# Optimization experiments

Measured on AMD Instinct MI355X. Metric: run time of the kernel, lower is better.

The kernel has to match this reference:

```python
import jax, jax.numpy as jnp
import numpy as np

B, S, IN, D, H, L, F = 4, 1024, 6, 512, 8, 4, 2048
DK = D // H
EPS = 1e-5

def _pos_encoding(S, D):
    pos = np.arange(S, dtype=np.float32)[:, None]
    div = np.exp(np.arange(0, D, 2, dtype=np.float32) * (-np.log(10000.0) / D))
    pe = np.zeros((S, D), np.float32)
    pe[:, 0::2] = np.sin(pos * div)
    pe[:, 1::2] = np.cos(pos * div)
    return jnp.asarray(pe)

def setup_inputs() -> dict:
    key = jax.random.key(0)
    ks = jax.random.split(key, 12)
    def w(k, shape):
        return jax.random.normal(k, shape, jnp.float32) * 0.02
    return {
        "left_wrist": jax.random.normal(ks[0], (B, S, IN), jnp.float32),
        "right_wrist": jax.random.normal(ks[1], (B, S, IN), jnp.float32),
        "Wl": w(ks[2], (IN, D)), "bl": jnp.zeros((D,), jnp.float32),
        "Wr": w(ks[3], (IN, D)), "br": jnp.zeros((D,), jnp.float32),
        "pe": _pos_encoding(S, D),
        # 4 attention blocks per layer (cross1to2, cross2to1, self1, self2), each with q/k/v/o projections
        "mha_w": w(ks[4], (L, 4, 4, D, D)), "mha_b": jnp.zeros((L, 4, 4, D), jnp.float32),
        "mha_ln_g": jnp.ones((L, 4, D), jnp.float32), "mha_ln_b": jnp.zeros((L, 4, D), jnp.float32),
        # 2 FFNs per layer (channel 1 / channel 2)
        "ff_w1": w(ks[5], (L, 2, D, F)), "ff_b1": jnp.zeros((L, 2, F), jnp.float32),
        "ff_w2": w(ks[6], (L, 2, F, D)), "ff_b2": jnp.zeros((L, 2, D), jnp.float32),
        "ff_ln_g": jnp.ones((L, 2, D), jnp.float32), "ff_ln_b": jnp.zeros((L, 2, D), jnp.float32),
        "h1_w1": w(ks[7], (2 * D, D)), "h1_b1": jnp.zeros((D,), jnp.float32),
        "h1_w2": w(ks[8], (D, 2)), "h1_b2": jnp.zeros((2,), jnp.float32),
        "h2_w1": w(ks[9], (2 * D, D)), "h2_b1": jnp.zeros((D,), jnp.float32),
        "h2_w2": w(ks[10], (D, 2)), "h2_b2": jnp.zeros((2,), jnp.float32),
    }

def _ln(x, g, b):
    m = jnp.mean(x, axis=-1, keepdims=True)
    v = jnp.var(x, axis=-1, keepdims=True)
    return (x - m) * jax.lax.rsqrt(v + EPS) * g + b

def _mha(q_in, k_in, v_in, w, b, g, beta):
    # w: [4, D, D] for q/k/v/o, b: [4, D]
    def proj(x, i):
        return (x @ w[i] + b[i]).reshape(x.shape[0], x.shape[1], H, DK).transpose(0, 2, 1, 3)
    Q, K, V = proj(q_in, 0), proj(k_in, 1), proj(v_in, 2)
    scores = jnp.einsum('bhqd,bhkd->bhqk', Q, K) * np.float32(1.0 / np.sqrt(DK))
    attn = jax.nn.softmax(scores, axis=-1)
    ctx = jnp.einsum('bhqk,bhkd->bhqd', attn, V)
    ctx = ctx.transpose(0, 2, 1, 3).reshape(q_in.shape[0], q_in.shape[1], D)
    out = ctx @ w[3] + b[3]
    return _ln(out + q_in, g, beta)

def _ffn(x, w1, b1, w2, b2, g, beta):
    h = jax.nn.relu(x @ w1 + b1)
    return _ln(h @ w2 + b2 + x, g, beta)

def reference(left_wrist, right_wrist, Wl, bl, Wr, br, pe,
              mha_w, mha_b, mha_ln_g, mha_ln_b,
              ff_w1, ff_b1, ff_w2, ff_b2, ff_ln_g, ff_ln_b,
              h1_w1, h1_b1, h1_w2, h1_b2, h2_w1, h2_b1, h2_w2, h2_b2):
    left = left_wrist @ Wl + bl + pe[None]
    right = right_wrist @ Wr + br + pe[None]
    for l in range(L):
        lc = _mha(left, right, right, mha_w[l, 0], mha_b[l, 0], mha_ln_g[l, 0], mha_ln_b[l, 0])
        rc = _mha(right, left, left, mha_w[l, 1], mha_b[l, 1], mha_ln_g[l, 1], mha_ln_b[l, 1])
        ls = _mha(lc, lc, lc, mha_w[l, 2], mha_b[l, 2], mha_ln_g[l, 2], mha_ln_b[l, 2])
        rs = _mha(rc, rc, rc, mha_w[l, 3], mha_b[l, 3], mha_ln_g[l, 3], mha_ln_b[l, 3])
        left = _ffn(ls, ff_w1[l, 0], ff_b1[l, 0], ff_w2[l, 0], ff_b2[l, 0], ff_ln_g[l, 0], ff_ln_b[l, 0])
        right = _ffn(rs, ff_w1[l, 1], ff_b1[l, 1], ff_w2[l, 1], ff_b2[l, 1], ff_ln_g[l, 1], ff_ln_b[l, 1])
    # AdaptiveAvgPool1d(1) over seq == mean over seq axis
    fused = jnp.concatenate([jnp.mean(left, axis=1), jnp.mean(right, axis=1)], axis=1)  # [B, 2D]
    logits1 = jax.nn.relu(fused @ h1_w1 + h1_b1) @ h1_w2 + h1_b2
    logits2 = jax.nn.relu(fused @ h2_w1 + h2_b1) @ h2_w2 + h2_b2
    return (logits1, logits2)
```

## Files before the change

kernel.cpp:

```cpp
#include <hip/hip_runtime.h>
#include <hip/hip_bf16.h>

#define NB 4
#define NS 1024
#define NIN 6
#define ND 512
#define NH 8
#define NLAYERS 4
#define NF 2048
#define NDK 64
#define LN_EPS 1e-5f

typedef unsigned short u16;
typedef __attribute__((ext_vector_type(4))) unsigned short u16x4;
typedef __attribute__((ext_vector_type(8))) short s16x8;
typedef __attribute__((ext_vector_type(4))) float f32x4;
typedef __attribute__((ext_vector_type(4))) unsigned int u32x4;

#define MFMA_BF16(A, B, C) __builtin_amdgcn_mfma_f32_16x16x32_bf16(A, B, C, 0, 0, 0)

#define GLOAD_LDS16(gsrc, ldst)                                                  \
    __builtin_amdgcn_global_load_lds(                                            \
        (const __attribute__((address_space(1))) void*)(gsrc),                   \
        (__attribute__((address_space(3))) void*)(ldst), 16, 0, 0)

__device__ inline u16 f2bf(float f) {
    __bf16 h = (__bf16)f;
    return __builtin_bit_cast(u16, h);
}
__device__ inline float bf2f(u16 v) {
    unsigned int u = (unsigned int)v << 16;
    return __builtin_bit_cast(float, u);
}

__global__ __launch_bounds__(256) void transpose_kernel(
    const float* __restrict__ src, u16* __restrict__ dst, int K, int N) {
    __shared__ u16 t[64][72];
    const int tid = threadIdx.x;
    src += (size_t)blockIdx.z * K * N;
    dst += (size_t)blockIdx.z * K * N;
    const int n0 = blockIdx.x * 64, k0 = blockIdx.y * 64;
    {
        int r = tid >> 2, cq = (tid & 3) * 16;
        const float* sp = src + (size_t)(k0 + r) * N + n0 + cq;
#pragma unroll
        for (int q = 0; q < 4; ++q) {
            float4 v = *reinterpret_cast<const float4*>(sp + q * 4);
            t[r][cq + q * 4 + 0] = f2bf(v.x);
            t[r][cq + q * 4 + 1] = f2bf(v.y);
            t[r][cq + q * 4 + 2] = f2bf(v.z);
            t[r][cq + q * 4 + 3] = f2bf(v.w);
        }
    }
    __syncthreads();
    {
        int rn = tid >> 2, cq = (tid & 3) * 16;
        s16x8 o0, o1;
#pragma unroll
        for (int j = 0; j < 8; ++j) o0[j] = (short)t[cq + j][rn];
#pragma unroll
        for (int j = 0; j < 8; ++j) o1[j] = (short)t[cq + 8 + j][rn];
        u16* dp = dst + (size_t)(n0 + rn) * K + k0 + cq;
        *reinterpret_cast<s16x8*>(dp) = o0;
        *reinterpret_cast<s16x8*>(dp + 8) = o1;
    }
}

__global__ __launch_bounds__(256) void in_proj_kernel(
    const float* __restrict__ x, const float* __restrict__ W,
    const float* __restrict__ bias, const float* __restrict__ pe,
    float* __restrict__ out, u16* __restrict__ outb) {
    int idx = blockIdx.x * 256 + threadIdx.x;
    int d = idx & (ND - 1);
    int bs = idx / ND;
    int s = bs & (NS - 1);
    const float* xr = x + (size_t)bs * NIN;
    float acc = bias[d] + pe[(size_t)s * ND + d];
#pragma unroll
    for (int i = 0; i < NIN; ++i) acc += xr[i] * W[(size_t)i * ND + d];
    out[idx] = acc;
    outb[idx] = f2bf(acc);
}

template <int BN>
__device__ inline void gemm_core(const u16* __restrict__ A, const u16* __restrict__ Wt,
                                 int K, int bm, int bn, char* lds, int tid,
                                 f32x4 (&acc)[4][BN / 32]) {
    constexpr int NT = BN / 32;
    constexpr int ASZ = 128 * 128;
    constexpr int BSZ = BN * 128;
    const int wid = tid >> 6, lane = tid & 63;
    const int l15 = lane & 15, lhi = lane >> 4;
    const int wr = wid >> 1, wc = wid & 1;

    auto stage = [&](int buf, int k0) {
#pragma unroll
        for (int i = 0; i < 4; ++i) {
            int slot = (wid * 4 + i) * 64 + lane;
            int r = slot >> 3, p = slot & 7;
            const char* src = (const char*)(A + (size_t)(bm + r) * K + k0)
                              + ((p * 16) ^ ((r & 7) << 4));
            GLOAD_LDS16(src, lds + buf * ASZ + (wid * 4 + i) * 1024);
        }
#pragma unroll
        for (int i = 0; i < BN / 32; ++i) {
            int slot = (wid * (BN / 32) + i) * 64 + lane;
            int r = slot >> 3, p = slot & 7;
            const char* src = (const char*)(Wt + (size_t)(bn + r) * K + k0)
                              + ((p * 16) ^ ((r & 7) << 4));
            GLOAD_LDS16(src, lds + 2 * ASZ + buf * BSZ + (wid * (BN / 32) + i) * 1024);
        }
    };

#pragma unroll
    for (int mt = 0; mt < 4; ++mt)
#pragma unroll
        for (int nt = 0; nt < NT; ++nt) acc[mt][nt] = f32x4{0.f, 0.f, 0.f, 0.f};

    const int KT = K >> 6;
    stage(0, 0);
    __syncthreads();
    for (int t = 0; t < KT; ++t) {
        if (t + 1 < KT) stage((t + 1) & 1, (t + 1) << 6);
        const char* Ab = lds + (t & 1) * ASZ;
        const char* Bb = lds + 2 * ASZ + (t & 1) * BSZ;
#pragma unroll
        for (int sl = 0; sl < 2; ++sl) {
            s16x8 af[4];
#pragma unroll
            for (int mt = 0; mt < 4; ++mt) {
                int row = wr * 64 + mt * 16 + l15;
                af[mt] = *reinterpret_cast<const s16x8*>(
                    Ab + ((row * 128 + sl * 64 + lhi * 16) ^ ((row & 7) << 4)));
            }
            s16x8 bfr[NT];
#pragma unroll
            for (int nt = 0; nt < NT; ++nt) {
                int row = wc * (BN / 2) + nt * 16 + l15;
                bfr[nt] = *reinterpret_cast<const s16x8*>(
                    Bb + ((row * 128 + sl * 64 + lhi * 16) ^ ((row & 7) << 4)));
            }
#pragma unroll
            for (int mt = 0; mt < 4; ++mt)
#pragma unroll
                for (int nt = 0; nt < NT; ++nt)
                    acc[mt][nt] = MFMA_BF16(af[mt], bfr[nt], acc[mt][nt]);
        }
        __syncthreads();
    }
}

template <int OMODE, int BN>
__global__ __launch_bounds__(256) void bgemm2_kernel(
    const u16* __restrict__ a0, const u16* __restrict__ a1,
    const u16* __restrict__ wt0, const u16* __restrict__ wt1,
    const float* __restrict__ bias0, const float* __restrict__ bias1,
    u16* __restrict__ Cv, int M, int N, int K) {
    constexpr int NT = BN / 32;
    __shared__ char lds[2 * 128 * 128 + 2 * BN * 128];
    const int tid = threadIdx.x, z = blockIdx.z;
    const int bm = blockIdx.y * 128, bn = blockIdx.x * BN;
    const u16* A = z ? a1 : a0;
    const u16* Wt = z ? wt1 : wt0;
    const float* bias = z ? bias1 : bias0;

    f32x4 acc[4][NT];
    gemm_core<BN>(A, Wt, K, bm, bn, lds, tid, acc);

    const int wid = tid >> 6, lane = tid & 63;
    const int l15 = lane & 15, lhi = lane >> 4;
    const int wr = wid >> 1, wc = wid & 1;
    float bv[NT];
#pragma unroll
    for (int nt = 0; nt < NT; ++nt) bv[nt] = bias[bn + wc * (BN / 2) + nt * 16 + l15];

    u16* C = Cv + (size_t)z * M * N;
#pragma unroll
    for (int mt = 0; mt < 4; ++mt) {
        int m0 = bm + wr * 64 + mt * 16 + lhi * 4;
#pragma unroll
        for (int nt = 0; nt < NT; ++nt) {
            int n = bn + wc * (BN / 2) + nt * 16 + l15;
#pragma unroll
            for (int r = 0; r < 4; ++r) {
                float v = acc[mt][nt][r] + bv[nt];
                if (OMODE == 1) v = fmaxf(v, 0.f);
                C[(size_t)(m0 + r) * N + n] = f2bf(v);
            }
        }
    }
}

__global__ __launch_bounds__(256) void bgemm_qkv_kernel(
    const u16* __restrict__ aq0, const u16* __restrict__ aq1,
    const u16* __restrict__ akv0, const u16* __restrict__ akv1,
    const u16* __restrict__ wt0, const u16* __restrict__ wt1,
    const float* __restrict__ bb0, const float* __restrict__ bb1,
    u16* __restrict__ Qo, u16* __restrict__ Ko, u16* __restrict__ Vto) {
    __shared__ char lds[2 * 128 * 128 + 2 * 64 * 128];
    const int tid = threadIdx.x, z = blockIdx.z;
    const int proj = blockIdx.x >> 3;
    const int bm = blockIdx.y * 128, bn = (blockIdx.x & 7) * 64;
    const int M = NB * NS;
    const u16* A = (proj == 0) ? (z ? aq1 : aq0) : (z ? akv1 : akv0);
    const u16* Wt = (z ? wt1 : wt0) + (size_t)proj * ND * ND;
    const float* bias = (z ? bb1 : bb0) + proj * ND;

    f32x4 acc[4][2];
    gemm_core<64>(A, Wt, ND, bm, bn, lds, tid, acc);

    const int wid = tid >> 6, lane = tid & 63;
    const int l15 = lane & 15, lhi = lane >> 4;
    const int wr = wid >> 1, wc = wid & 1;
    float bv[2];
#pragma unroll
    for (int nt = 0; nt < 2; ++nt) bv[nt] = bias[bn + wc * 32 + nt * 16 + l15];

    if (proj < 2) {
        u16* C = (proj ? Ko : Qo) + (size_t)z * M * ND;
#pragma unroll
        for (int mt = 0; mt < 4; ++mt) {
            int m0 = bm + wr * 64 + mt * 16 + lhi * 4;
#pragma unroll
            for (int nt = 0; nt < 2; ++nt) {
                int n = bn + wc * 32 + nt * 16 + l15;
#pragma unroll
                for (int r = 0; r < 4; ++r)
                    C[(size_t)(m0 + r) * ND + n] = f2bf(acc[mt][nt][r] + bv[nt]);
            }
        }
    } else {
#pragma unroll
        for (int mt = 0; mt < 4; ++mt) {
            int m0 = bm + wr * 64 + mt * 16 + lhi * 4;
            int b = (z * M + m0) >> 10, s = m0 & (NS - 1);
#pragma unroll
            for (int nt = 0; nt < 2; ++nt) {
                int n = bn + wc * 32 + nt * 16 + l15;
                int h = n >> 6, dk = n & 63;
                u16x4 o = {f2bf(acc[mt][nt][0] + bv[nt]), f2bf(acc[mt][nt][1] + bv[nt]),
                           f2bf(acc[mt][nt][2] + bv[nt]), f2bf(acc[mt][nt][3] + bv[nt])};
                *reinterpret_cast<u16x4*>(Vto + ((size_t)((b * NH + h) * NDK + dk)) * NS + s) = o;
            }
        }
    }
}

__global__ __launch_bounds__(256) void ln2_kernel(
    const u16* __restrict__ x, const float* __restrict__ res,
    const float* __restrict__ g0, const float* __restrict__ g1,
    const float* __restrict__ be0, const float* __restrict__ be1,
    float* __restrict__ outf, u16* __restrict__ outb) {
    const int wid = threadIdx.x >> 6, lane = threadIdx.x & 63;
    const int row = blockIdx.x * 4 + wid;
    const float* g = (row >> 12) ? g1 : g0;
    const float* be = (row >> 12) ? be1 : be0;
    const int c0 = lane * 8;
    const size_t base = (size_t)row * ND + c0;

    u32x4 xp = *reinterpret_cast<const u32x4*>(x + base);
    float4 ra = *reinterpret_cast<const float4*>(res + base);
    float4 rb = *reinterpret_cast<const float4*>(res + base + 4);
    float v[8];
    v[0] = bf2f((u16)(xp[0] & 0xffffu)) + ra.x;
    v[1] = bf2f((u16)(xp[0] >> 16)) + ra.y;
    v[2] = bf2f((u16)(xp[1] & 0xffffu)) + ra.z;
    v[3] = bf2f((u16)(xp[1] >> 16)) + ra.w;
    v[4] = bf2f((u16)(xp[2] & 0xffffu)) + rb.x;
    v[5] = bf2f((u16)(xp[2] >> 16)) + rb.y;
    v[6] = bf2f((u16)(xp[3] & 0xffffu)) + rb.z;
    v[7] = bf2f((u16)(xp[3] >> 16)) + rb.w;

    float s = 0.f, sq = 0.f;
#pragma unroll
    for (int i = 0; i < 8; ++i) { s += v[i]; sq += v[i] * v[i]; }
#pragma unroll
    for (int m = 1; m < 64; m <<= 1) { s += __shfl_xor(s, m); sq += __shfl_xor(sq, m); }
    float mean = s * (1.f / ND);
    float var = sq * (1.f / ND) - mean * mean;
    float rstd = rsqrtf(var + LN_EPS);

    float4 ga = *reinterpret_cast<const float4*>(g + c0);
    float4 gb = *reinterpret_cast<const float4*>(g + c0 + 4);
    float4 ba = *reinterpret_cast<const float4*>(be + c0);
    float4 bb = *reinterpret_cast<const float4*>(be + c0 + 4);
    float gg[8] = {ga.x, ga.y, ga.z, ga.w, gb.x, gb.y, gb.z, gb.w};
    float bbv[8] = {ba.x, ba.y, ba.z, ba.w, bb.x, bb.y, bb.z, bb.w};
    float o[8];
#pragma unroll
    for (int i = 0; i < 8; ++i) o[i] = (v[i] - mean) * rstd * gg[i] + bbv[i];

    float4 oa = {o[0], o[1], o[2], o[3]};
    float4 ob = {o[4], o[5], o[6], o[7]};
    *reinterpret_cast<float4*>(outf + base) = oa;
    *reinterpret_cast<float4*>(outf + base + 4) = ob;
    u32x4 pk;
#pragma unroll
    for (int i = 0; i < 4; ++i)
        pk[i] = (unsigned int)f2bf(o[2 * i]) | ((unsigned int)f2bf(o[2 * i + 1]) << 16);
    *reinterpret_cast<u32x4*>(outb + base) = pk;
}

__global__ __launch_bounds__(256, 4) void attn_kernel(
    const u16* __restrict__ Qb, const u16* __restrict__ Kb,
    const u16* __restrict__ Vtb, u16* __restrict__ O) {
    __shared__ u16 Ks[128 * 64];
    __shared__ u16 Vts[64 * 128];
    __shared__ u16 Ps[4][16 * 64];

    const int tid = threadIdx.x;
    const int w = tid >> 6, lane = tid & 63;
    const int l15 = lane & 15, lhi = lane >> 4;
    const int bh = blockIdx.y;
    const int b = bh >> 3, h = bh & 7;
    const int qb = blockIdx.x * 64 + w * 16;
    const float c1 = 0.18033688011f;

    s16x8 qf[2];
    {
        const u16* qp = Qb + ((size_t)(b * NS) + qb + l15) * ND + h * NDK + lhi * 8;
        qf[0] = *reinterpret_cast<const s16x8*>(qp);
        qf[1] = *reinterpret_cast<const s16x8*>(qp + 32);
    }

    f32x4 o[4] = {f32x4{0.f, 0.f, 0.f, 0.f}, f32x4{0.f, 0.f, 0.f, 0.f},
                  f32x4{0.f, 0.f, 0.f, 0.f}, f32x4{0.f, 0.f, 0.f, 0.f}};
    float m = -1e30f;
    float lsum = 0.f;

    const u16* Kbase = Kb + ((size_t)(b * NS)) * ND + h * NDK;
    const u16* Vbase = Vtb + ((size_t)bh * NDK) * NS;

    for (int c = 0; c < NS / 128; ++c) {
        const int kv0 = c * 128;
        __syncthreads();
#pragma unroll
        for (int i = 0; i < 4; ++i) {
            int slot = (w * 4 + i) * 64 + lane;
            {
                int r = slot >> 3, p = slot & 7;
                const char* src = (const char*)(Kbase + (size_t)(kv0 + r) * ND)
                                  + ((p ^ (r & 7)) * 16);
                GLOAD_LDS16(src, (char*)Ks + (w * 4 + i) * 1024);
            }
            {
                int r = slot >> 4, p = slot & 15;
                const char* src = (const char*)(Vbase + (size_t)r * NS + kv0)
                                  + ((p ^ (r & 7)) * 16);
                GLOAD_LDS16(src, (char*)Vts + (w * 4 + i) * 1024);
            }
        }
        __syncthreads();

        f32x4 sc[8];
#pragma unroll
        for (int blk = 0; blk < 8; ++blk) sc[blk] = f32x4{0.f, 0.f, 0.f, 0.f};
#pragma unroll
        for (int sl = 0; sl < 2; ++sl) {
#pragma unroll
            for (int blk = 0; blk < 8; ++blk) {
                int krow = blk * 16 + l15;
                s16x8 kf = *reinterpret_cast<const s16x8*>((char*)Ks +
                    ((krow * 128 + sl * 64 + lhi * 16) ^ ((krow & 7) << 4)));
                sc[blk] = MFMA_BF16(kf, qf[sl], sc[blk]);
            }
        }
        float mx = -1e30f;
#pragma unroll
        for (int blk = 0; blk < 8; ++blk)
#pragma unroll
            for (int r = 0; r < 4; ++r) mx = fmaxf(mx, sc[blk][r]);
        mx = fmaxf(mx, __shfl_xor(mx, 16));
        mx = fmaxf(mx, __shfl_xor(mx, 32));
        float mn = fmaxf(m, mx);
        if (__any((mn - m) * c1 > 8.f)) {
            float corr = exp2f((m - mn) * c1);
            m = mn;
            lsum *= corr;
            float cO[4];
#pragma unroll
            for (int r = 0; r < 4; ++r) cO[r] = __shfl(corr, lhi * 4 + r);
#pragma unroll
            for (int db = 0; db < 4; ++db)
#pragma unroll
                for (int r = 0; r < 4; ++r) o[db][r] *= cO[r];
        }
        float d = m * c1;
        float rs = 0.f;
#pragma unroll
        for (int blk = 0; blk < 8; ++blk) {
#pragma unroll
            for (int r = 0; r < 4; ++r) {
                float p = exp2f(fmaf(sc[blk][r], c1, -d));
                sc[blk][r] = p;
                rs += p;
            }
        }
        rs += __shfl_xor(rs, 16);
        rs += __shfl_xor(rs, 32);
        lsum += rs;

#pragma unroll
        for (int hh = 0; hh < 2; ++hh) {
#pragma unroll
            for (int bl = 0; bl < 4; ++bl) {
                int blk = hh * 4 + bl;
                u16x4 pk = {f2bf(sc[blk][0]), f2bf(sc[blk][1]),
                            f2bf(sc[blk][2]), f2bf(sc[blk][3])};
                *reinterpret_cast<u16x4*>((char*)(Ps[w]) +
                    ((l15 * 128 + bl * 32 + lhi * 8) ^ ((l15 & 7) << 4))) = pk;
            }
#pragma unroll
            for (int sl2 = 0; sl2 < 2; ++sl2) {
                s16x8 pf = *reinterpret_cast<const s16x8*>((char*)(Ps[w]) +
                    ((l15 * 128 + sl2 * 64 + lhi * 16) ^ ((l15 & 7) << 4)));
                int ss = hh * 2 + sl2;
#pragma unroll
                for (int db = 0; db < 4; ++db) {
                    int vr = db * 16 + l15;
                    s16x8 vf = *reinterpret_cast<const s16x8*>((char*)Vts +
                        ((vr * 256 + ss * 64 + lhi * 16) ^ ((vr & 7) << 4)));
                    o[db] = MFMA_BF16(pf, vf, o[db]);
                }
            }
        }
    }
    float lsO[4];
#pragma unroll
    for (int r = 0; r < 4; ++r) lsO[r] = __shfl(lsum, lhi * 4 + r);
#pragma unroll
    for (int db = 0; db < 4; ++db) {
#pragma unroll
        for (int r = 0; r < 4; ++r) {
            int q = qb + lhi * 4 + r;
            O[((size_t)(b * NS) + q) * ND + h * NDK + db * 16 + l15] =
                f2bf(o[db][r] / lsO[r]);
        }
    }
}

__global__ __launch_bounds__(256) void pool2_kernel(
    const float* __restrict__ RES, float* __restrict__ fused) {
    const int b = blockIdx.x, half = blockIdx.y, sc = blockIdx.z;
    const size_t NTOK = (size_t)NB * NS * ND;
    const float* src = RES + (half ? NTOK : 0) + ((size_t)(b * NS + sc * 128)) * ND;
    const int tid = threadIdx.x;
#pragma unroll
    for (int cc = 0; cc < 2; ++cc) {
        int c = cc * 256 + tid;
        float s = 0.f;
        for (int r = 0; r < 128; ++r) s += src[(size_t)r * ND + c];
        atomicAdd(&fused[b * 1024 + half * 512 + c], s * (1.f / NS));
    }
}

__global__ __launch_bounds__(256) void head_hidden_kernel(
    const float* __restrict__ fused,
    const float* __restrict__ w1a, const float* __restrict__ b1a,
    const float* __restrict__ w1b, const float* __restrict__ b1b,
    float* __restrict__ hid) {
    const int b = blockIdx.x >> 1, head = blockIdx.x & 1;
    const float* w1 = head ? w1b : w1a;
    const float* b1 = head ? b1b : b1a;
    const int tid = threadIdx.x;
    const int j = blockIdx.y * 64 + (tid & 63);
    const int kq = tid >> 6;
    const float* fr = fused + (size_t)b * (2 * ND);
    float p = 0.f;
    for (int k = kq * 256; k < kq * 256 + 256; ++k)
        p += fr[k] * w1[(size_t)k * ND + j];
    __shared__ float part[4][64];
    part[kq][tid & 63] = p;
    __syncthreads();
    if (tid < 64) {
        float v = part[0][tid] + part[1][tid] + part[2][tid] + part[3][tid] + b1[j];
        hid[(size_t)blockIdx.x * ND + j] = fmaxf(v, 0.f);
    }
}

__global__ __launch_bounds__(256) void head_out_kernel(
    const float* __restrict__ hid,
    const float* __restrict__ w2a, const float* __restrict__ b2a,
    const float* __restrict__ w2b, const float* __restrict__ b2b,
    float* __restrict__ out) {
    const int b = blockIdx.x >> 1, head = blockIdx.x & 1;
    const float* w2 = head ? w2b : w2a;
    const float* b2 = head ? b2b : b2a;
    const int tid = threadIdx.x;
    const float* hr = hid + (size_t)blockIdx.x * ND;
    float h0 = hr[tid], h1 = hr[tid + 256];
    float p0 = h0 * w2[tid * 2 + 0] + h1 * w2[(tid + 256) * 2 + 0];
    float p1 = h0 * w2[tid * 2 + 1] + h1 * w2[(tid + 256) * 2 + 1];
#pragma unroll
    for (int m = 1; m < 64; m <<= 1) { p0 += __shfl_xor(p0, m); p1 += __shfl_xor(p1, m); }
    __shared__ float r0s[4], r1s[4];
    int wid = tid >> 6, lane = tid & 63;
    if (lane == 0) { r0s[wid] = p0; r1s[wid] = p1; }
    __syncthreads();
    if (tid == 0) {
        out[head * 8 + b * 2 + 0] = r0s[0] + r0s[1] + r0s[2] + r0s[3] + b2[0];
        out[head * 8 + b * 2 + 1] = r1s[0] + r1s[1] + r1s[2] + r1s[3] + b2[1];
    }
}

extern "C" void kernel_launch(void* const* d_in, const int* in_sizes, int n_in,
                              void* d_out, int out_size, void* d_ws, size_t ws_size,
                              hipStream_t stream) {
    const float* left_wrist  = (const float*)d_in[0];
    const float* right_wrist = (const float*)d_in[1];
    const float* Wl = (const float*)d_in[2];
    const float* bl = (const float*)d_in[3];
    const float* Wr = (const float*)d_in[4];
    const float* br = (const float*)d_in[5];
    const float* pe = (const float*)d_in[6];
    const float* mha_w    = (const float*)d_in[7];
    const float* mha_b    = (const float*)d_in[8];
    const float* mha_ln_g = (const float*)d_in[9];
    const float* mha_ln_b = (const float*)d_in[10];
    const float* ff_w1 = (const float*)d_in[11];
    const float* ff_b1 = (const float*)d_in[12];
    const float* ff_w2 = (const float*)d_in[13];
    const float* ff_b2 = (const float*)d_in[14];
    const float* ff_ln_g = (const float*)d_in[15];
    const float* ff_ln_b = (const float*)d_in[16];
    const float* h1_w1 = (const float*)d_in[17];
    const float* h1_b1 = (const float*)d_in[18];
    const float* h1_w2 = (const float*)d_in[19];
    const float* h1_b2 = (const float*)d_in[20];
    const float* h2_w1 = (const float*)d_in[21];
    const float* h2_b1 = (const float*)d_in[22];
    const float* h2_w2 = (const float*)d_in[23];
    const float* h2_b2 = (const float*)d_in[24];
    float* out = (float*)d_out;

    const size_t NTOK = (size_t)NB * NS * ND;
    const int M = NB * NS;
    float* ws = (float*)d_ws;
    float* RES   = ws;
    float* CRES  = RES + 2 * NTOK;
    float* TMPf  = CRES + 2 * NTOK;
    float* FUSED = TMPf + 2 * NTOK;
    float* HID   = FUSED + NB * 2 * ND;
    u16* TMPbf = (u16*)TMPf;
    u16* Xbf  = (u16*)(HID + 8 * ND);
    u16* CXbf = Xbf + 2 * NTOK;
    u16* Qbf  = CXbf + 2 * NTOK;
    u16* Kbf  = Qbf + 2 * NTOK;
    u16* Vtbf = Kbf + 2 * NTOK;
    u16* CTbf = Vtbf + 2 * NTOK;
    u16* Hh   = Qbf;
    u16* WtM  = CTbf + 2 * NTOK;
    u16* WtF1 = WtM + (size_t)64 * ND * ND;
    u16* WtF2 = WtF1 + (size_t)8 * ND * NF;

    const size_t DD = (size_t)ND * ND;

    transpose_kernel<<<dim3(ND / 64, ND / 64, 64), 256, 0, stream>>>(mha_w, WtM, ND, ND);
    transpose_kernel<<<dim3(NF / 64, ND / 64, 8), 256, 0, stream>>>(ff_w1, WtF1, ND, NF);
    transpose_kernel<<<dim3(ND / 64, NF / 64, 8), 256, 0, stream>>>(ff_w2, WtF2, NF, ND);

    in_proj_kernel<<<(NB * NS * ND) / 256, 256, 0, stream>>>(left_wrist, Wl, bl, pe, RES, Xbf);
    in_proj_kernel<<<(NB * NS * ND) / 256, 256, 0, stream>>>(right_wrist, Wr, br, pe,
                                                             RES + NTOK, Xbf + NTOK);

    for (int l = 0; l < NLAYERS; ++l) {
        const u16* wt0 = WtM + ((size_t)l * 4 + 0) * 4 * DD;
        const u16* wt1 = WtM + ((size_t)l * 4 + 1) * 4 * DD;
        const u16* wt2 = WtM + ((size_t)l * 4 + 2) * 4 * DD;
        const u16* wt3 = WtM + ((size_t)l * 4 + 3) * 4 * DD;
        const float* bb0 = mha_b + ((size_t)l * 4 + 0) * 4 * ND;
        const float* bb1 = mha_b + ((size_t)l * 4 + 1) * 4 * ND;
        const float* bb2 = mha_b + ((size_t)l * 4 + 2) * 4 * ND;
        const float* bb3 = mha_b + ((size_t)l * 4 + 3) * 4 * ND;

        bgemm_qkv_kernel<<<dim3(24, 32, 2), 256, 0, stream>>>(
            Xbf, Xbf + NTOK, Xbf + NTOK, Xbf, wt0, wt1, bb0, bb1, Qbf, Kbf, Vtbf);
        attn_kernel<<<dim3(NS / 64, 2 * NB * NH), 256, 0, stream>>>(Qbf, Kbf, Vtbf, CTbf);
        bgemm2_kernel<2, 64><<<dim3(8, 32, 2), 256, 0, stream>>>(
            CTbf, CTbf + NTOK, wt0 + 3 * DD, wt1 + 3 * DD, bb0 + 3 * ND, bb1 + 3 * ND,
            TMPbf, M, ND, ND);
        ln2_kernel<<<2 * M / 4, 256, 0, stream>>>(
            TMPbf, RES, mha_ln_g + ((size_t)l * 4 + 0) * ND, mha_ln_g + ((size_t)l * 4 + 1) * ND,
            mha_ln_b + ((size_t)l * 4 + 0) * ND, mha_ln_b + ((size_t)l * 4 + 1) * ND,
            CRES, CXbf);

        bgemm_qkv_kernel<<<dim3(24, 32, 2), 256, 0, stream>>>(
            CXbf, CXbf + NTOK, CXbf, CXbf + NTOK, wt2, wt3, bb2, bb3, Qbf, Kbf, Vtbf);
        attn_kernel<<<dim3(NS / 64, 2 * NB * NH), 256, 0, stream>>>(Qbf, Kbf, Vtbf, CTbf);
        bgemm2_kernel<2, 64><<<dim3(8, 32, 2), 256, 0, stream>>>(
            CTbf, CTbf + NTOK, wt2 + 3 * DD, wt3 + 3 * DD, bb2 + 3 * ND, bb3 + 3 * ND,
            TMPbf, M, ND, ND);
        ln2_kernel<<<2 * M / 4, 256, 0, stream>>>(
            TMPbf, CRES, mha_ln_g + ((size_t)l * 4 + 2) * ND, mha_ln_g + ((size_t)l * 4 + 3) * ND,
            mha_ln_b + ((size_t)l * 4 + 2) * ND, mha_ln_b + ((size_t)l * 4 + 3) * ND,
            RES, Xbf);

        bgemm2_kernel<1, 128><<<dim3(16, 32, 2), 256, 0, stream>>>(
            Xbf, Xbf + NTOK, WtF1 + ((size_t)l * 2 + 0) * ND * NF, WtF1 + ((size_t)l * 2 + 1) * ND * NF,
            ff_b1 + ((size_t)l * 2 + 0) * NF, ff_b1 + ((size_t)l * 2 + 1) * NF,
            Hh, M, NF, ND);
        bgemm2_kernel<2, 64><<<dim3(8, 32, 2), 256, 0, stream>>>(
            Hh, Hh + (size_t)M * NF, WtF2 + ((size_t)l * 2 + 0) * NF * ND, WtF2 + ((size_t)l * 2 + 1) * NF * ND,
            ff_b2 + ((size_t)l * 2 + 0) * ND, ff_b2 + ((size_t)l * 2 + 1) * ND,
            TMPbf, M, ND, NF);
        ln2_kernel<<<2 * M / 4, 256, 0, stream>>>(
            TMPbf, RES, ff_ln_g + ((size_t)l * 2 + 0) * ND, ff_ln_g + ((size_t)l * 2 + 1) * ND,
            ff_ln_b + ((size_t)l * 2 + 0) * ND, ff_ln_b + ((size_t)l * 2 + 1) * ND,
            RES, Xbf);
    }

    hipMemsetAsync(FUSED, 0, NB * 2 * ND * sizeof(float), stream);
    pool2_kernel<<<dim3(NB, 2, 8), 256, 0, stream>>>(RES, FUSED);
    head_hidden_kernel<<<dim3(8, 8), 256, 0, stream>>>(FUSED, h1_w1, h1_b1, h2_w1, h2_b1, HID);
    head_out_kernel<<<8, 256, 0, stream>>>(HID, h1_w2, h1_b2, h2_w2, h2_b2, out);
}
```

Before: 1.320 ms.

## Widen attention blocks to 8 waves, remap grid, and stage output through LDS

The attention kernel now runs 512 threads (8 waves, 128 queries per block), so each K/V chunk loaded into LDS is shared by twice as many query rows. The 1-D grid index is remapped so that consecutive blocks land on different batch-head pairs, which is likely meant to spread load across XCDs or L2 slices. The output is written into the per-wave P buffer first and then stored as 16-byte row-contiguous vectors instead of scattered 2-byte stores. The cost is fewer blocks (512) and higher per-block LDS and register pressure.

```diff
diff --git a/kernel.cpp b/kernel.cpp
--- a/kernel.cpp
+++ b/kernel.cpp
@@ -301,19 +301,21 @@
     *reinterpret_cast<u32x4*>(outb + base) = pk;
 }
 
-__global__ __launch_bounds__(256, 4) void attn_kernel(
+__global__ __launch_bounds__(512, 6) void attn_kernel(
     const u16* __restrict__ Qb, const u16* __restrict__ Kb,
     const u16* __restrict__ Vtb, u16* __restrict__ O) {
     __shared__ u16 Ks[128 * 64];
     __shared__ u16 Vts[64 * 128];
-    __shared__ u16 Ps[4][16 * 64];
+    __shared__ u16 Ps[8][16 * 64];
 
     const int tid = threadIdx.x;
     const int w = tid >> 6, lane = tid & 63;
     const int l15 = lane & 15, lhi = lane >> 4;
-    const int bh = blockIdx.y;
+    const int i0 = blockIdx.x;
+    const int qx = (i0 >> 3) & 7;
+    const int bh = (i0 & 7) * 8 + (i0 >> 6);
     const int b = bh >> 3, h = bh & 7;
-    const int qb = blockIdx.x * 64 + w * 16;
+    const int qb = qx * 128 + w * 16;
     const float c1 = 0.18033688011f;
 
     s16x8 qf[2];
@@ -335,19 +337,19 @@
         const int kv0 = c * 128;
         __syncthreads();
 #pragma unroll
-        for (int i = 0; i < 4; ++i) {
-            int slot = (w * 4 + i) * 64 + lane;
+        for (int i = 0; i < 2; ++i) {
+            int slot = i * 512 + tid;
             {
                 int r = slot >> 3, p = slot & 7;
                 const char* src = (const char*)(Kbase + (size_t)(kv0 + r) * ND)
                                   + ((p ^ (r & 7)) * 16);
-                GLOAD_LDS16(src, (char*)Ks + (w * 4 + i) * 1024);
+                GLOAD_LDS16(src, (char*)Ks + (i * 512 + w * 64) * 16);
             }
             {
                 int r = slot >> 4, p = slot & 15;
                 const char* src = (const char*)(Vbase + (size_t)r * NS + kv0)
                                   + ((p ^ (r & 7)) * 16);
-                GLOAD_LDS16(src, (char*)Vts + (w * 4 + i) * 1024);
+                GLOAD_LDS16(src, (char*)Vts + (i * 512 + w * 64) * 16);
             }
         }
         __syncthreads();
@@ -429,13 +431,17 @@
 #pragma unroll
     for (int r = 0; r < 4; ++r) lsO[r] = __shfl(lsum, lhi * 4 + r);
 #pragma unroll
-    for (int db = 0; db < 4; ++db) {
-#pragma unroll
-        for (int r = 0; r < 4; ++r) {
-            int q = qb + lhi * 4 + r;
-            O[((size_t)(b * NS) + q) * ND + h * NDK + db * 16 + l15] =
-                f2bf(o[db][r] / lsO[r]);
-        }
+    for (int db = 0; db < 4; ++db)
+#pragma unroll
+        for (int r = 0; r < 4; ++r)
+            Ps[w][(lhi * 4 + r) * 64 + db * 16 + l15] = f2bf(o[db][r] / lsO[r]);
+    u16* Obase = O + ((size_t)(b * NS) + qb) * ND + h * NDK;
+#pragma unroll
+    for (int it = 0; it < 2; ++it) {
+        int slot = it * 64 + lane;
+        int row = slot >> 3, col8 = (slot & 7) * 8;
+        *reinterpret_cast<s16x8*>(Obase + (size_t)row * ND + col8) =
+            *reinterpret_cast<const s16x8*>(Ps[w] + row * 64 + col8);
     }
 }
 
@@ -575,7 +581,7 @@
 
         bgemm_qkv_kernel<<<dim3(24, 32, 2), 256, 0, stream>>>(
             Xbf, Xbf + NTOK, Xbf + NTOK, Xbf, wt0, wt1, bb0, bb1, Qbf, Kbf, Vtbf);
-        attn_kernel<<<dim3(NS / 64, 2 * NB * NH), 256, 0, stream>>>(Qbf, Kbf, Vtbf, CTbf);
+        attn_kernel<<<dim3(512), 512, 0, stream>>>(Qbf, Kbf, Vtbf, CTbf);
         bgemm2_kernel<2, 64><<<dim3(8, 32, 2), 256, 0, stream>>>(
             CTbf, CTbf + NTOK, wt0 + 3 * DD, wt1 + 3 * DD, bb0 + 3 * ND, bb1 + 3 * ND,
             TMPbf, M, ND, ND);
@@ -586,7 +592,7 @@
 
         bgemm_qkv_kernel<<<dim3(24, 32, 2), 256, 0, stream>>>(
             CXbf, CXbf + NTOK, CXbf, CXbf + NTOK, wt2, wt3, bb2, bb3, Qbf, Kbf, Vtbf);
-        attn_kernel<<<dim3(NS / 64, 2 * NB * NH), 256, 0, stream>>>(Qbf, Kbf, Vtbf, CTbf);
+        attn_kernel<<<dim3(512), 512, 0, stream>>>(Qbf, Kbf, Vtbf, CTbf);
         bgemm2_kernel<2, 64><<<dim3(8, 32, 2), 256, 0, stream>>>(
             CTbf, CTbf + NTOK, wt2 + 3 * DD, wt3 + 3 * DD, bb2 + 3 * ND, bb3 + 3 * ND,
             TMPbf, M, ND, ND);
```

New measurement: 1.811 ms. +37.2%, slower.
